# Kernel optimization log

Hardware: AMD Instinct MI355X
Metric: run time of the kernel (lower is better)

Reference implementation:

```python
import jax, jax.numpy as jnp
import numpy as np

N_NODES = 150000
D = 64
N_EDGES = 2000000  # bidirectional: 2 * num_train_edges


def setup_inputs() -> dict:
    key = jax.random.key(0)
    k1, k2, k3, k4, k5 = jax.random.split(key, 5)
    nodes_emb = jax.random.normal(k1, (N_NODES, D), dtype=jnp.float32)
    src = jax.random.randint(k2, (N_EDGES,), 0, N_NODES, dtype=jnp.int64 if jax.config.jax_enable_x64 else jnp.int32).astype(jnp.int32)
    dst = jax.random.randint(k3, (N_EDGES,), 0, N_NODES, dtype=jnp.int32)
    W1 = jax.random.normal(k4, (2 * D, D), dtype=jnp.float32) * (1.0 / np.sqrt(2 * D))
    b1 = jnp.zeros((D,), dtype=jnp.float32)
    W2 = jax.random.normal(k5, (D, 1), dtype=jnp.float32) * (1.0 / np.sqrt(D))
    b2 = jnp.zeros((1,), dtype=jnp.float32)
    return {"nodes_emb": nodes_emb, "src": src, "dst": dst,
            "W1": W1, "b1": b1, "W2": W2, "b2": b2}


def reference(nodes_emb, src, dst, W1, b1, W2, b2):
    # Gather per-edge endpoint embeddings and concat: [E, 2D]
    emb_src = nodes_emb[src]          # [E, D]
    emb_dst = nodes_emb[dst]          # [E, D]
    edge_emb = jnp.concatenate([emb_src, emb_dst], axis=1)  # [E, 2D]
    # 2-layer MLP edge scorer: Linear(2D->D) -> ReLU -> Linear(D->1)
    h = jax.nn.relu(edge_emb @ W1 + b1)  # [E, D]
    edge_logits = h @ W2 + b2            # [E, 1]
    return edge_logits
```

## Files before the change

kernel.cpp:

```cpp
#include <hip/hip_runtime.h>
#include <math.h>

typedef __attribute__((ext_vector_type(8))) short bf16x8;
typedef __attribute__((ext_vector_type(4))) float f32x4;
typedef __attribute__((ext_vector_type(2))) unsigned int u32x2;
typedef __attribute__((ext_vector_type(4))) unsigned int u32x4;
typedef unsigned long long u64;

#define LDSTR 136
#define TPW 8
#define NREP 128
#define NBKT 64

static __device__ __forceinline__ unsigned int pack2bf(float x, float y) {
  unsigned int ux = __builtin_bit_cast(unsigned int, x);
  ux += 0x7fffu + ((ux >> 16) & 1u);
  unsigned int uy = __builtin_bit_cast(unsigned int, y);
  uy += 0x7fffu + ((uy >> 16) & 1u);
  return (ux >> 16) | (uy & 0xffff0000u);
}
static __device__ __forceinline__ unsigned short f2bf_s(float x) {
  unsigned int ux = __builtin_bit_cast(unsigned int, x);
  ux += 0x7fffu + ((ux >> 16) & 1u);
  return (unsigned short)(ux >> 16);
}
static __device__ __forceinline__ bf16x8 make_afrag(float4 lo, float4 hi) {
  u32x4 p;
  p[0] = pack2bf(lo.x, lo.y);
  p[1] = pack2bf(lo.z, lo.w);
  p[2] = pack2bf(hi.x, hi.y);
  p[3] = pack2bf(hi.z, hi.w);
  return __builtin_bit_cast(bf16x8, p);
}

static __device__ __forceinline__ unsigned int q8(float v, float inv) {
  return (unsigned int)((int)rintf(v * inv) + 128);
}

static __device__ __forceinline__ float dot8i(u32x2 P, u32x2 Q, float sp, float sq,
                                              const float* w2v) {
  const float t_ = -128.f * (sp + sq);
  float acc = 0.f;
  #pragma unroll
  for (int k2 = 0; k2 < 2; ++k2) {
    const unsigned int pd = P[k2], qd = Q[k2];
    #pragma unroll
    for (int b = 0; b < 4; ++b) {
      float pf = (float)((pd >> (8 * b)) & 0xffu);
      float qf = (float)((qd >> (8 * b)) & 0xffu);
      float h = __builtin_fmaf(pf, sp, __builtin_fmaf(qf, sq, t_));
      h = fmaxf(h, 0.f);
      acc = __builtin_fmaf(h, w2v[k2 * 4 + b], acc);
    }
  }
  return acc;
}

__global__ __launch_bounds__(256) void node_proj(
    const float* __restrict__ emb,
    const float* __restrict__ W1,
    const float* __restrict__ b1,
    unsigned int* __restrict__ P8,
    unsigned int* __restrict__ Q8,
    float* __restrict__ SP,
    float* __restrict__ SQ,
    int N, int ntiles)
{
  __shared__ unsigned short ls_w1t[64 * LDSTR];
  const int tid  = threadIdx.x;
  const int wave = tid >> 6;
  const int lane = tid & 63;
  const int l15  = lane & 15;
  const int quad = lane >> 4;

  for (int i = tid; i < 64 * 128; i += 256) {
    int k = i >> 6, n = i & 63;
    ls_w1t[n * LDSTR + k] = f2bf_s(W1[i]);
  }
  __syncthreads();

  float b1q[4];
  #pragma unroll
  for (int tn = 0; tn < 4; ++tn) b1q[tn] = b1[tn * 16 + l15];

  bf16x8 bfragP[4][2], bfragQ[4][2];
  #pragma unroll
  for (int tn = 0; tn < 4; ++tn)
    #pragma unroll
    for (int s = 0; s < 2; ++s) {
      bfragP[tn][s] = *(const bf16x8*)&ls_w1t[(tn * 16 + l15) * LDSTR + s * 32 + quad * 8];
      bfragQ[tn][s] = *(const bf16x8*)&ls_w1t[(tn * 16 + l15) * LDSTR + 64 + s * 32 + quad * 8];
    }

  for (int tile = blockIdx.x * 4 + wave; tile < ntiles; tile += gridDim.x * 4) {
    const int base = tile * 16;

    bf16x8 afr0, afr1;
    {
      int node = base + l15;
      node = (node < N) ? node : N - 1;
      const float* rp = emb + (long long)node * 64 + quad * 8;
      afr0 = make_afrag(*(const float4*)(rp),      *(const float4*)(rp + 4));
      afr1 = make_afrag(*(const float4*)(rp + 32), *(const float4*)(rp + 36));
    }

    f32x4 aP[4], aQ[4];
    #pragma unroll
    for (int tn = 0; tn < 4; ++tn) { aP[tn] = (f32x4){0,0,0,0}; aQ[tn] = (f32x4){0,0,0,0}; }
    #pragma unroll
    for (int tn = 0; tn < 4; ++tn) {
      aP[tn] = __builtin_amdgcn_mfma_f32_16x16x32_bf16(afr0, bfragP[tn][0], aP[tn], 0, 0, 0);
      aQ[tn] = __builtin_amdgcn_mfma_f32_16x16x32_bf16(afr0, bfragQ[tn][0], aQ[tn], 0, 0, 0);
      aP[tn] = __builtin_amdgcn_mfma_f32_16x16x32_bf16(afr1, bfragP[tn][1], aP[tn], 0, 0, 0);
      aQ[tn] = __builtin_amdgcn_mfma_f32_16x16x32_bf16(afr1, bfragQ[tn][1], aQ[tn], 0, 0, 0);
    }

    #pragma unroll
    for (int r = 0; r < 4; ++r) {
      const int m = base + quad * 4 + r;
      float vp0 = aP[0][r], vp1 = aP[1][r], vp2 = aP[2][r], vp3 = aP[3][r];
      float vq0 = aQ[0][r] + b1q[0], vq1 = aQ[1][r] + b1q[1];
      float vq2 = aQ[2][r] + b1q[2], vq3 = aQ[3][r] + b1q[3];

      float mp = fmaxf(fmaxf(fabsf(vp0), fabsf(vp1)), fmaxf(fabsf(vp2), fabsf(vp3)));
      float mq = fmaxf(fmaxf(fabsf(vq0), fabsf(vq1)), fmaxf(fabsf(vq2), fabsf(vq3)));
      mp = fmaxf(mp, __shfl_xor(mp, 1)); mq = fmaxf(mq, __shfl_xor(mq, 1));
      mp = fmaxf(mp, __shfl_xor(mp, 2)); mq = fmaxf(mq, __shfl_xor(mq, 2));
      mp = fmaxf(mp, __shfl_xor(mp, 4)); mq = fmaxf(mq, __shfl_xor(mq, 4));
      mp = fmaxf(mp, __shfl_xor(mp, 8)); mq = fmaxf(mq, __shfl_xor(mq, 8));

      const float invP = (mp > 0.f) ? 127.f / mp : 0.f;
      const float invQ = (mq > 0.f) ? 127.f / mq : 0.f;

      if (m < N) {
        unsigned int pw = q8(vp0, invP) | (q8(vp1, invP) << 8) |
                          (q8(vp2, invP) << 16) | (q8(vp3, invP) << 24);
        unsigned int qw = q8(vq0, invQ) | (q8(vq1, invQ) << 8) |
                          (q8(vq2, invQ) << 16) | (q8(vq3, invQ) << 24);
        P8[(long long)m * 16 + l15] = pw;
        Q8[(long long)m * 16 + l15] = qw;
        if (l15 == 0) {
          SP[m] = mp * (1.f / 127.f);
          SQ[m] = mq * (1.f / 127.f);
        }
      }
    }
  }
}

__global__ __launch_bounds__(256) void bucketize(
    const int* __restrict__ src, const int* __restrict__ dst,
    unsigned int* __restrict__ seg, unsigned short* __restrict__ posrec,
    unsigned int* __restrict__ cntT,
    int E, int ndiv, int cap)
{
  __shared__ unsigned int curs[NBKT];
  const int r = blockIdx.x;
  const int per = (E + NREP - 1) / NREP;
  const int lo = r * per;
  const int hi = (lo + per < E) ? lo + per : E;
  for (int i = threadIdx.x; i < NBKT; i += 256) curs[i] = 0;
  __syncthreads();
  for (int e = lo + threadIdx.x; e < hi; e += 256) {
    const int s = src[e], d = dst[e];
    const int bi = s / ndiv, bj = d / ndiv;
    const int bkt = bi * 8 + bj;
    const unsigned int pos = atomicAdd(&curs[bkt], 1u);
    unsigned short pr = 0xFFFFu;
    if (pos < (unsigned)cap) {
      seg[((size_t)(r * NBKT + bkt)) * cap + pos] =
          (unsigned)(s - bi * ndiv) | ((unsigned)(d - bj * ndiv) << 15);
      pr = (unsigned short)(((unsigned)bkt << 9) | pos);
    }
    posrec[e] = pr;
  }
  __syncthreads();
  for (int bkt = threadIdx.x; bkt < NBKT; bkt += 256) {
    unsigned int c = curs[bkt];
    cntT[bkt * NREP + r] = (c < (unsigned)cap) ? c : (unsigned)cap;
  }
}

__global__ __launch_bounds__(256) void edge_score_seg(
    const unsigned int* __restrict__ P8, const unsigned int* __restrict__ Q8,
    const float* __restrict__ SP, const float* __restrict__ SQ,
    const unsigned int* __restrict__ seg, const unsigned int* __restrict__ cntT,
    const float* __restrict__ W2, const float* __restrict__ b2,
    float* __restrict__ tmp, int cap, int ndiv)
{
  const int tid  = threadIdx.x;
  const int lane = tid & 63;
  const int sv   = lane & 7;
  const int g    = lane >> 3;
  const int k    = blockIdx.x & 7;
  const int tblk = blockIdx.x >> 3;
  const int wgid = tblk * 4 + (tid >> 6);
  const int r    = wgid >> 3;
  const int sub  = wgid & 7;

  float w2v[8];
  #pragma unroll
  for (int j = 0; j < 8; ++j) {
    const int pos = sv * 8 + j;
    const int ch  = (pos & 3) * 16 + (pos >> 2);
    w2v[j] = W2[ch];
  }
  const float b2v = b2[0];
  const int sd = sv * 2;
  const int sbase = k * ndiv;

  #pragma unroll 1
  for (int j = 0; j < 8; ++j) {
    const int b = k * 8 + j;
    const int dbase = j * ndiv;
    const int cnt = (int)cntT[b * NREP + r];
    const int chunk = (cnt + 7) >> 3;
    const int lo = sub * chunk;
    const int hi = (cnt < lo + chunk) ? cnt : lo + chunk;
    const unsigned int* sgp = seg + (size_t)(r * NBKT + b) * cap;
    float* tp = tmp + (size_t)(r * NBKT + b) * cap;

    #pragma unroll 2
    for (int m = lo + g; m < hi; m += 8) {
      const unsigned int v = sgp[m];
      const int s_ = sbase + (int)(v & 0x7FFFu);
      const int d_ = dbase + (int)(v >> 15);

      const u32x2 pv = *(const u32x2*)(P8 + s_ * 16 + sd);
      const u32x2 qv = *(const u32x2*)(Q8 + d_ * 16 + sd);
      const float sp = SP[s_], sq = SQ[d_];

      float acc = dot8i(pv, qv, sp, sq, w2v);
      acc += __shfl_xor(acc, 1);
      acc += __shfl_xor(acc, 2);
      acc += __shfl_xor(acc, 4);
      if (sv == 0) tp[m] = acc + b2v;
    }
  }
}

__global__ __launch_bounds__(256) void unscatter(
    const unsigned short* __restrict__ posrec, const float* __restrict__ tmp,
    float* __restrict__ out,
    const int* __restrict__ src, const int* __restrict__ dst,
    const unsigned int* __restrict__ P8, const unsigned int* __restrict__ Q8,
    const float* __restrict__ SP, const float* __restrict__ SQ,
    const float* __restrict__ W2, const float* __restrict__ b2,
    int E, int per, int cap)
{
  const int r   = blockIdx.x >> 3;
  const int sub = blockIdx.x & 7;
  const int lo_r = r * per;
  int lenr = E - lo_r;
  if (lenr <= 0) return;
  if (lenr > per) lenr = per;
  const int chunk = (lenr + 7) >> 3;
  const int lo = lo_r + sub * chunk;
  int hi = lo + chunk;
  const int end_r = lo_r + lenr;
  if (hi > end_r) hi = end_r;
  const float* tb = tmp + (size_t)r * NBKT * cap;

  for (int e = lo + threadIdx.x; e < hi; e += 256) {
    const unsigned int pr = posrec[e];
    if (pr != 0xFFFFu) {
      out[e] = tb[(pr >> 9) * cap + (pr & 511u)];
    } else {
      const int s_ = src[e], d_ = dst[e];
      const float sp = SP[s_], sq = SQ[d_];
      const float t_ = -128.f * (sp + sq);
      float acc = 0.f;
      for (int w = 0; w < 16; ++w) {
        const unsigned int pd = P8[(size_t)s_ * 16 + w];
        const unsigned int qd = Q8[(size_t)d_ * 16 + w];
        for (int bb = 0; bb < 4; ++bb) {
          const int pos = w * 4 + bb;
          const int ch  = (pos & 3) * 16 + (pos >> 2);
          float pf = (float)((pd >> (8 * bb)) & 0xffu);
          float qf = (float)((qd >> (8 * bb)) & 0xffu);
          float h = __builtin_fmaf(pf, sp, __builtin_fmaf(qf, sq, t_));
          h = fmaxf(h, 0.f);
          acc = __builtin_fmaf(h, W2[ch], acc);
        }
      }
      out[e] = acc + b2[0];
    }
  }
}

__global__ __launch_bounds__(256) void edge_score(
    const unsigned int* __restrict__ P8, const unsigned int* __restrict__ Q8,
    const float* __restrict__ SP, const float* __restrict__ SQ,
    const int* __restrict__ src, const int* __restrict__ dst,
    const float* __restrict__ W2, const float* __restrict__ b2,
    float* __restrict__ out, int E)
{
  const int tid  = blockIdx.x * 256 + threadIdx.x;
  const int lane = threadIdx.x & 63;
  const int s    = lane & 7;
  const int g    = lane >> 3;
  const int wid  = tid >> 6;
  const int step = gridDim.x * 4 * 32;

  float w2v[8];
  #pragma unroll
  for (int j = 0; j < 8; ++j) {
    const int pos = s * 8 + j;
    const int ch  = (pos & 3) * 16 + (pos >> 2);
    w2v[j] = W2[ch];
  }
  const float b2v = b2[0];
  const int sd = s * 2;

  int e0 = wid * 32;
  if (e0 >= E) return;

  int iA, iB, iC, iD, jA, jB, jC, jD;
  {
    const int eA = e0 + g,      eAc = (eA < E) ? eA : E - 1;
    const int eB = e0 + 8 + g,  eBc = (eB < E) ? eB : E - 1;
    const int eC = e0 + 16 + g, eCc = (eC < E) ? eC : E - 1;
    const int eD = e0 + 24 + g, eDc = (eD < E) ? eD : E - 1;
    iA = src[eAc]; jA = dst[eAc];
    iB = src[eBc]; jB = dst[eBc];
    iC = src[eCc]; jC = dst[eCc];
    iD = src[eDc]; jD = dst[eDc];
  }
  float spA = SP[iA], sqA = SQ[jA];
  float spB = SP[iB], sqB = SQ[jB];
  float spC = SP[iC], sqC = SQ[jC];
  float spD = SP[iD], sqD = SQ[jD];

  while (true) {
    const u32x2 pA = *(const u32x2*)(P8 + iA * 16 + sd);
    const u32x2 qA = *(const u32x2*)(Q8 + jA * 16 + sd);
    const u32x2 pB = *(const u32x2*)(P8 + iB * 16 + sd);
    const u32x2 qB = *(const u32x2*)(Q8 + jB * 16 + sd);
    const u32x2 pC = *(const u32x2*)(P8 + iC * 16 + sd);
    const u32x2 qC = *(const u32x2*)(Q8 + jC * 16 + sd);
    const u32x2 pD = *(const u32x2*)(P8 + iD * 16 + sd);
    const u32x2 qD = *(const u32x2*)(Q8 + jD * 16 + sd);

    const int en = e0 + step;
    const bool more = (en < E);
    int nA = iA, nB = iB, nC = iC, nD = iD;
    int mA = jA, mB = jB, mC = jC, mD = jD;
    if (more) {
      const int fA = en + g,      fAc = (fA < E) ? fA : E - 1;
      const int fB = en + 8 + g,  fBc = (fB < E) ? fB : E - 1;
      const int fC = en + 16 + g, fCc = (fC < E) ? fC : E - 1;
      const int fD = en + 24 + g, fDc = (fD < E) ? fD : E - 1;
      nA = src[fAc]; mA = dst[fAc];
      nB = src[fBc]; mB = dst[fBc];
      nC = src[fCc]; mC = dst[fCc];
      nD = src[fDc]; mD = dst[fDc];
    }

    float accA = dot8i(pA, qA, spA, sqA, w2v);
    float accB = dot8i(pB, qB, spB, sqB, w2v);
    float accC = dot8i(pC, qC, spC, sqC, w2v);
    float accD = dot8i(pD, qD, spD, sqD, w2v);

    accA += __shfl_xor(accA, 1); accB += __shfl_xor(accB, 1);
    accC += __shfl_xor(accC, 1); accD += __shfl_xor(accD, 1);
    accA += __shfl_xor(accA, 2); accB += __shfl_xor(accB, 2);
    accC += __shfl_xor(accC, 2); accD += __shfl_xor(accD, 2);
    accA += __shfl_xor(accA, 4); accB += __shfl_xor(accB, 4);
    accC += __shfl_xor(accC, 4); accD += __shfl_xor(accD, 4);

    if (s == 0) {
      const int eA = e0 + g;
      const int eB = e0 + 8 + g;
      const int eC = e0 + 16 + g;
      const int eD = e0 + 24 + g;
      if (eA < E) out[eA] = accA + b2v;
      if (eB < E) out[eB] = accB + b2v;
      if (eC < E) out[eC] = accC + b2v;
      if (eD < E) out[eD] = accD + b2v;
    }

    if (!more) break;
    iA = nA; iB = nB; iC = nC; iD = nD;
    jA = mA; jB = mB; jC = mC; jD = mD;
    spA = SP[iA]; sqA = SQ[jA];
    spB = SP[iB]; sqB = SQ[jB];
    spC = SP[iC]; sqC = SQ[jC];
    spD = SP[iD]; sqD = SQ[jD];
    e0 = en;
  }
}

__global__ __launch_bounds__(256) void edge_mlp_f32(
    const float* __restrict__ nodes_emb, const int* __restrict__ src,
    const int* __restrict__ dst, const float* __restrict__ W1,
    const float* __restrict__ b1, const float* __restrict__ W2,
    const float* __restrict__ b2, float* __restrict__ out, int E)
{
  __shared__ unsigned short ls_w1t[64 * LDSTR];
  __shared__ float ls_b1[64];
  __shared__ float ls_w2[64];
  const int tid = threadIdx.x, wave = tid >> 6, lane = tid & 63;
  const int l15 = lane & 15, quad = lane >> 4;
  for (int i = tid; i < 64 * 128; i += 256) {
    int n = i >> 7, k = i & 127;
    ls_w1t[n * LDSTR + k] = f2bf_s(W1[k * 64 + n]);
  }
  if (tid < 64) { ls_b1[tid] = b1[tid]; ls_w2[tid] = W2[tid]; }
  __syncthreads();
  bf16x8 bfrag[4][4];
  #pragma unroll
  for (int tn = 0; tn < 4; ++tn)
    #pragma unroll
    for (int s = 0; s < 4; ++s)
      bfrag[tn][s] = *(const bf16x8*)&ls_w1t[(tn * 16 + l15) * LDSTR + s * 32 + quad * 8];
  float myb1[4], myw2[4];
  #pragma unroll
  for (int tn = 0; tn < 4; ++tn) { myb1[tn] = ls_b1[tn*16+l15]; myw2[tn] = ls_w2[tn*16+l15]; }
  const float b2v = b2[0];
  const int wave_base = blockIdx.x * (TPW * 64) + wave * (TPW * 16);
  #pragma unroll 1
  for (int t = 0; t < TPW; ++t) {
    const int tile_base = wave_base + t * 16;
    if (tile_base >= E) break;
    const int e = tile_base + l15;
    const int si = src[e], di = dst[e];
    const float* srow = nodes_emb + (long long)si * 64 + quad * 8;
    const float* drow = nodes_emb + (long long)di * 64 + quad * 8;
    float4 v0 = *(const float4*)(srow),      v1 = *(const float4*)(srow + 4);
    float4 v2 = *(const float4*)(srow + 32), v3 = *(const float4*)(srow + 36);
    float4 v4 = *(const float4*)(drow),      v5 = *(const float4*)(drow + 4);
    float4 v6 = *(const float4*)(drow + 32), v7 = *(const float4*)(drow + 36);
    bf16x8 afr[4] = {make_afrag(v0,v1), make_afrag(v2,v3), make_afrag(v4,v5), make_afrag(v6,v7)};
    f32x4 acc[4];
    #pragma unroll
    for (int tn = 0; tn < 4; ++tn) acc[tn] = (f32x4){0.f,0.f,0.f,0.f};
    #pragma unroll
    for (int s = 0; s < 4; ++s)
      #pragma unroll
      for (int tn = 0; tn < 4; ++tn)
        acc[tn] = __builtin_amdgcn_mfma_f32_16x16x32_bf16(afr[s], bfrag[tn][s], acc[tn], 0, 0, 0);
    #pragma unroll
    for (int r = 0; r < 4; ++r) {
      float p = 0.f;
      #pragma unroll
      for (int tn = 0; tn < 4; ++tn) {
        float h = fmaxf(acc[tn][r] + myb1[tn], 0.f);
        p = __builtin_fmaf(h, myw2[tn], p);
      }
      p += __shfl_xor(p, 1); p += __shfl_xor(p, 2);
      p += __shfl_xor(p, 4); p += __shfl_xor(p, 8);
      if (l15 == 0) out[tile_base + quad * 4 + r] = p + b2v;
    }
  }
}

extern "C" void kernel_launch(void* const* d_in, const int* in_sizes, int n_in,
                              void* d_out, int out_size, void* d_ws, size_t ws_size,
                              hipStream_t stream) {
  const float* nodes_emb = (const float*)d_in[0];
  const int*   src       = (const int*)d_in[1];
  const int*   dst       = (const int*)d_in[2];
  const float* W1        = (const float*)d_in[3];
  const float* b1        = (const float*)d_in[4];
  const float* W2        = (const float*)d_in[5];
  const float* b2        = (const float*)d_in[6];
  float* out = (float*)d_out;

  const int E = in_sizes[1];
  const int nodes_elems = in_sizes[0];
  const int N = nodes_elems / 64;
  const int ntiles = (N + 15) / 16;
  const int ndiv = (N + 7) / 8;
  const int per  = (E + NREP - 1) / NREP;

  const long long cells = (long long)NBKT * NREP;
  const int perCell = (int)((E + cells - 1) / cells);
  const int sig = (int)ceilf(sqrtf((float)(perCell > 0 ? perCell : 1)));
  const int cap = perCell + 6 * sig + 8;

  const size_t szRow   = (size_t)N * 64;
  const size_t offSP   = szRow * 2;
  const size_t offSQ   = offSP + (size_t)N * 4;
  const size_t offCnt  = offSQ + (size_t)N * 4;
  const size_t offPos  = offCnt + (size_t)NBKT * NREP * 4;
  const size_t offSeg  = (offPos + (size_t)E * 2 + 7) & ~(size_t)7;
  const size_t offTmp  = offSeg + (size_t)NBKT * NREP * (size_t)cap * 4;
  const size_t need_full = offTmp + (size_t)NBKT * NREP * (size_t)cap * 4;
  const size_t need_mid  = offCnt;

  if (ws_size >= need_mid && N > 0) {
    unsigned int* P8 = (unsigned int*)d_ws;
    unsigned int* Q8 = (unsigned int*)((char*)d_ws + szRow);
    float* SP = (float*)((char*)d_ws + offSP);
    float* SQ = (float*)((char*)d_ws + offSQ);
    hipLaunchKernelGGL(node_proj, dim3(512), dim3(256), 0, stream,
                       nodes_emb, W1, b1, P8, Q8, SP, SQ, N, ntiles);
    if (ws_size >= need_full && cap <= 511 && ndiv <= 32767) {
      unsigned int*  cntT   = (unsigned int*)((char*)d_ws + offCnt);
      unsigned short* posrec = (unsigned short*)((char*)d_ws + offPos);
      unsigned int*  seg    = (unsigned int*)((char*)d_ws + offSeg);
      float*         tmp    = (float*)((char*)d_ws + offTmp);
      hipLaunchKernelGGL(bucketize, dim3(NREP), dim3(256), 0, stream,
                         src, dst, seg, posrec, cntT, E, ndiv, cap);
      hipLaunchKernelGGL(edge_score_seg, dim3(2048), dim3(256), 0, stream,
                         P8, Q8, SP, SQ, seg, cntT, W2, b2, tmp, cap, ndiv);
      hipLaunchKernelGGL(unscatter, dim3(NREP * 8), dim3(256), 0, stream,
                         posrec, tmp, out, src, dst, P8, Q8, SP, SQ, W2, b2,
                         E, per, cap);
    } else {
      hipLaunchKernelGGL(edge_score, dim3(4096), dim3(256), 0, stream,
                         P8, Q8, SP, SQ, src, dst, W2, b2, out, E);
    }
  } else {
    const int epb = TPW * 64;
    const int blocks = (E + epb - 1) / epb;
    hipLaunchKernelGGL(edge_mlp_f32, dim3(blocks), dim3(256), 0, stream,
                       nodes_emb, src, dst, W1, b1, W2, b2, out, E);
  }
}
```

Before: 205.8 us.

## Fuse node projection and bucketize into one launch; prefetch next edge in scorer

Merges the independent node_proj and bucketize kernels into a single fused_prep launch, with blocks split by index, so the two phases run concurrently and one launch boundary disappears. The edge scoring loop now software-pipelines its gathers, loading the next edge's P8/Q8/scale values before computing the current one, and it preloads the per-bucket counts into registers. The fused kernel's shared memory footprint is the larger of the two bodies, which may reduce occupancy, and the prefetch raises register pressure.

```diff
diff --git a/kernel.cpp b/kernel.cpp
--- a/kernel.cpp
+++ b/kernel.cpp
@@ -11,6 +11,7 @@
 #define TPW 8
 #define NREP 128
 #define NBKT 64
+#define PROJ_BLOCKS 512
 
 static __device__ __forceinline__ unsigned int pack2bf(float x, float y) {
   unsigned int ux = __builtin_bit_cast(unsigned int, x);
@@ -56,15 +57,12 @@
   return acc;
 }
 
-__global__ __launch_bounds__(256) void node_proj(
-    const float* __restrict__ emb,
-    const float* __restrict__ W1,
+static __device__ void node_proj_body(
+    const float* __restrict__ emb, const float* __restrict__ W1,
     const float* __restrict__ b1,
-    unsigned int* __restrict__ P8,
-    unsigned int* __restrict__ Q8,
-    float* __restrict__ SP,
-    float* __restrict__ SQ,
-    int N, int ntiles)
+    unsigned int* __restrict__ P8, unsigned int* __restrict__ Q8,
+    float* __restrict__ SP, float* __restrict__ SQ,
+    int N, int ntiles, int nblocks, int bid)
 {
   __shared__ unsigned short ls_w1t[64 * LDSTR];
   const int tid  = threadIdx.x;
@@ -92,7 +90,7 @@
       bfragQ[tn][s] = *(const bf16x8*)&ls_w1t[(tn * 16 + l15) * LDSTR + 64 + s * 32 + quad * 8];
     }
 
-  for (int tile = blockIdx.x * 4 + wave; tile < ntiles; tile += gridDim.x * 4) {
+  for (int tile = bid * 4 + wave; tile < ntiles; tile += nblocks * 4) {
     const int base = tile * 16;
 
     bf16x8 afr0, afr1;
@@ -148,14 +146,12 @@
   }
 }
 
-__global__ __launch_bounds__(256) void bucketize(
+static __device__ void bucketize_body(
     const int* __restrict__ src, const int* __restrict__ dst,
     unsigned int* __restrict__ seg, unsigned short* __restrict__ posrec,
-    unsigned int* __restrict__ cntT,
-    int E, int ndiv, int cap)
+    unsigned int* __restrict__ cntT, int E, int ndiv, int cap, int r)
 {
   __shared__ unsigned int curs[NBKT];
-  const int r = blockIdx.x;
   const int per = (E + NREP - 1) / NREP;
   const int lo = r * per;
   const int hi = (lo + per < E) ? lo + per : E;
@@ -181,6 +177,31 @@
   }
 }
 
+__global__ __launch_bounds__(256) void fused_prep(
+    const float* __restrict__ emb, const float* __restrict__ W1,
+    const float* __restrict__ b1,
+    unsigned int* __restrict__ P8, unsigned int* __restrict__ Q8,
+    float* __restrict__ SP, float* __restrict__ SQ,
+    const int* __restrict__ src, const int* __restrict__ dst,
+    unsigned int* __restrict__ seg, unsigned short* __restrict__ posrec,
+    unsigned int* __restrict__ cntT,
+    int N, int ntiles, int E, int ndiv, int cap)
+{
+  if (blockIdx.x < PROJ_BLOCKS)
+    node_proj_body(emb, W1, b1, P8, Q8, SP, SQ, N, ntiles, PROJ_BLOCKS, blockIdx.x);
+  else
+    bucketize_body(src, dst, seg, posrec, cntT, E, ndiv, cap, blockIdx.x - PROJ_BLOCKS);
+}
+
+__global__ __launch_bounds__(256) void node_proj(
+    const float* __restrict__ emb, const float* __restrict__ W1,
+    const float* __restrict__ b1,
+    unsigned int* __restrict__ P8, unsigned int* __restrict__ Q8,
+    float* __restrict__ SP, float* __restrict__ SQ, int N, int ntiles)
+{
+  node_proj_body(emb, W1, b1, P8, Q8, SP, SQ, N, ntiles, gridDim.x, blockIdx.x);
+}
+
 __global__ __launch_bounds__(256) void edge_score_seg(
     const unsigned int* __restrict__ P8, const unsigned int* __restrict__ Q8,
     const float* __restrict__ SP, const float* __restrict__ SQ,
@@ -209,32 +230,52 @@
   const int sd = sv * 2;
   const int sbase = k * ndiv;
 
+  int cnts[8];
+  #pragma unroll
+  for (int j = 0; j < 8; ++j) cnts[j] = (int)cntT[(k * 8 + j) * NREP + r];
+
   #pragma unroll 1
   for (int j = 0; j < 8; ++j) {
     const int b = k * 8 + j;
     const int dbase = j * ndiv;
-    const int cnt = (int)cntT[b * NREP + r];
+    const int cnt = cnts[j];
     const int chunk = (cnt + 7) >> 3;
     const int lo = sub * chunk;
     const int hi = (cnt < lo + chunk) ? cnt : lo + chunk;
     const unsigned int* sgp = seg + (size_t)(r * NBKT + b) * cap;
     float* tp = tmp + (size_t)(r * NBKT + b) * cap;
 
-    #pragma unroll 2
-    for (int m = lo + g; m < hi; m += 8) {
-      const unsigned int v = sgp[m];
-      const int s_ = sbase + (int)(v & 0x7FFFu);
-      const int d_ = dbase + (int)(v >> 15);
-
-      const u32x2 pv = *(const u32x2*)(P8 + s_ * 16 + sd);
-      const u32x2 qv = *(const u32x2*)(Q8 + d_ * 16 + sd);
-      const float sp = SP[s_], sq = SQ[d_];
+    int m = lo + g;
+    if (m >= hi) continue;
+
+    unsigned int v = sgp[m];
+    int s_ = sbase + (int)(v & 0x7FFFu);
+    int d_ = dbase + (int)(v >> 15);
+    u32x2 pv = *(const u32x2*)(P8 + s_ * 16 + sd);
+    u32x2 qv = *(const u32x2*)(Q8 + d_ * 16 + sd);
+    float sp = SP[s_], sq = SQ[d_];
+
+    while (true) {
+      const int m2 = m + 8;
+      const bool more = (m2 < hi);
+      u32x2 pv2, qv2; float sp2 = 0.f, sq2 = 0.f;
+      if (more) {
+        const unsigned int vn = sgp[m2];
+        const int s2 = sbase + (int)(vn & 0x7FFFu);
+        const int d2 = dbase + (int)(vn >> 15);
+        pv2 = *(const u32x2*)(P8 + s2 * 16 + sd);
+        qv2 = *(const u32x2*)(Q8 + d2 * 16 + sd);
+        sp2 = SP[s2]; sq2 = SQ[d2];
+      }
 
       float acc = dot8i(pv, qv, sp, sq, w2v);
       acc += __shfl_xor(acc, 1);
       acc += __shfl_xor(acc, 2);
       acc += __shfl_xor(acc, 4);
       if (sv == 0) tp[m] = acc + b2v;
+
+      if (!more) break;
+      m = m2; pv = pv2; qv = qv2; sp = sp2; sq = sq2;
     }
   }
 }
@@ -493,21 +534,22 @@
     unsigned int* Q8 = (unsigned int*)((char*)d_ws + szRow);
     float* SP = (float*)((char*)d_ws + offSP);
     float* SQ = (float*)((char*)d_ws + offSQ);
-    hipLaunchKernelGGL(node_proj, dim3(512), dim3(256), 0, stream,
-                       nodes_emb, W1, b1, P8, Q8, SP, SQ, N, ntiles);
     if (ws_size >= need_full && cap <= 511 && ndiv <= 32767) {
-      unsigned int*  cntT   = (unsigned int*)((char*)d_ws + offCnt);
+      unsigned int*   cntT   = (unsigned int*)((char*)d_ws + offCnt);
       unsigned short* posrec = (unsigned short*)((char*)d_ws + offPos);
-      unsigned int*  seg    = (unsigned int*)((char*)d_ws + offSeg);
-      float*         tmp    = (float*)((char*)d_ws + offTmp);
-      hipLaunchKernelGGL(bucketize, dim3(NREP), dim3(256), 0, stream,
-                         src, dst, seg, posrec, cntT, E, ndiv, cap);
+      unsigned int*   seg    = (unsigned int*)((char*)d_ws + offSeg);
+      float*          tmp    = (float*)((char*)d_ws + offTmp);
+      hipLaunchKernelGGL(fused_prep, dim3(PROJ_BLOCKS + NREP), dim3(256), 0, stream,
+                         nodes_emb, W1, b1, P8, Q8, SP, SQ,
+                         src, dst, seg, posrec, cntT, N, ntiles, E, ndiv, cap);
       hipLaunchKernelGGL(edge_score_seg, dim3(2048), dim3(256), 0, stream,
                          P8, Q8, SP, SQ, seg, cntT, W2, b2, tmp, cap, ndiv);
       hipLaunchKernelGGL(unscatter, dim3(NREP * 8), dim3(256), 0, stream,
                          posrec, tmp, out, src, dst, P8, Q8, SP, SQ, W2, b2,
                          E, per, cap);
     } else {
+      hipLaunchKernelGGL(node_proj, dim3(512), dim3(256), 0, stream,
+                         nodes_emb, W1, b1, P8, Q8, SP, SQ, N, ntiles);
       hipLaunchKernelGGL(edge_score, dim3(4096), dim3(256), 0, stream,
                          P8, Q8, SP, SQ, src, dst, W2, b2, out, E);
     }
```

Result: no change. 206.6 us (+0.4%).

## Pack per-node scales into bucket records and unroll bucketize edge loop

Applied to the files above, without the earlier changes.

Bucketize now gathers the SP/SQ scales for each edge and stores them as bf16 next to the packed index pair, in an 8-byte record. This moves the scattered scale loads out of edge_score_seg and into the sequential bucketing pass. The bucketize loop is unrolled four ways so several src/dst loads and scale gathers are in flight at once. edge_score_seg also preloads its bucket counts and skips empty ranges, and the overflow capacity margin is reduced. In exchange, the segment buffer doubles in size, the scales lose precision by rounding to bf16, and the tighter capacity raises the chance of overflow into the fallback path.

```diff
diff --git a/kernel.cpp b/kernel.cpp
--- a/kernel.cpp
+++ b/kernel.cpp
@@ -57,14 +57,10 @@
 }
 
 __global__ __launch_bounds__(256) void node_proj(
-    const float* __restrict__ emb,
-    const float* __restrict__ W1,
+    const float* __restrict__ emb, const float* __restrict__ W1,
     const float* __restrict__ b1,
-    unsigned int* __restrict__ P8,
-    unsigned int* __restrict__ Q8,
-    float* __restrict__ SP,
-    float* __restrict__ SQ,
-    int N, int ntiles)
+    unsigned int* __restrict__ P8, unsigned int* __restrict__ Q8,
+    float* __restrict__ SP, float* __restrict__ SQ, int N, int ntiles)
 {
   __shared__ unsigned short ls_w1t[64 * LDSTR];
   const int tid  = threadIdx.x;
@@ -150,9 +146,9 @@
 
 __global__ __launch_bounds__(256) void bucketize(
     const int* __restrict__ src, const int* __restrict__ dst,
-    unsigned int* __restrict__ seg, unsigned short* __restrict__ posrec,
-    unsigned int* __restrict__ cntT,
-    int E, int ndiv, int cap)
+    const float* __restrict__ SP, const float* __restrict__ SQ,
+    u32x2* __restrict__ seg, unsigned short* __restrict__ posrec,
+    unsigned int* __restrict__ cntT, int E, int ndiv, int cap)
 {
   __shared__ unsigned int curs[NBKT];
   const int r = blockIdx.x;
@@ -161,18 +157,43 @@
   const int hi = (lo + per < E) ? lo + per : E;
   for (int i = threadIdx.x; i < NBKT; i += 256) curs[i] = 0;
   __syncthreads();
-  for (int e = lo + threadIdx.x; e < hi; e += 256) {
-    const int s = src[e], d = dst[e];
-    const int bi = s / ndiv, bj = d / ndiv;
-    const int bkt = bi * 8 + bj;
-    const unsigned int pos = atomicAdd(&curs[bkt], 1u);
-    unsigned short pr = 0xFFFFu;
-    if (pos < (unsigned)cap) {
-      seg[((size_t)(r * NBKT + bkt)) * cap + pos] =
-          (unsigned)(s - bi * ndiv) | ((unsigned)(d - bj * ndiv) << 15);
-      pr = (unsigned short)(((unsigned)bkt << 9) | pos);
-    }
-    posrec[e] = pr;
+
+  for (int e0 = lo + threadIdx.x; e0 < hi; e0 += 1024) {
+    const int e1 = e0 + 256, e2 = e0 + 512, e3 = e0 + 768;
+    const int e1c = (e1 < hi) ? e1 : hi - 1;
+    const int e2c = (e2 < hi) ? e2 : hi - 1;
+    const int e3c = (e3 < hi) ? e3 : hi - 1;
+    const int s0 = src[e0],  d0 = dst[e0];
+    const int s1 = src[e1c], d1 = dst[e1c];
+    const int s2 = src[e2c], d2 = dst[e2c];
+    const int s3 = src[e3c], d3 = dst[e3c];
+    const float sp0 = SP[s0], sq0 = SQ[d0];
+    const float sp1 = SP[s1], sq1 = SQ[d1];
+    const float sp2 = SP[s2], sq2 = SQ[d2];
+    const float sp3 = SP[s3], sq3 = SQ[d3];
+
+#define BK_PROC(EE, SS, DD, SPV, SQV)                                         \
+    {                                                                         \
+      const int bi = (SS) / ndiv, bj = (DD) / ndiv;                           \
+      const int bkt = bi * 8 + bj;                                            \
+      const unsigned int pos = atomicAdd(&curs[bkt], 1u);                     \
+      unsigned short pr = 0xFFFFu;                                            \
+      if (pos < (unsigned)cap) {                                              \
+        u32x2 ev;                                                             \
+        ev[0] = (unsigned)((SS) - bi * ndiv) |                                \
+                ((unsigned)((DD) - bj * ndiv) << 15);                         \
+        ev[1] = ((unsigned)f2bf_s(SPV) << 16) | (unsigned)f2bf_s(SQV);        \
+        seg[((size_t)(r * NBKT + bkt)) * cap + pos] = ev;                     \
+        pr = (unsigned short)(((unsigned)bkt << 9) | pos);                    \
+      }                                                                       \
+      posrec[EE] = pr;                                                        \
+    }
+
+    BK_PROC(e0, s0, d0, sp0, sq0);
+    if (e1 < hi) BK_PROC(e1, s1, d1, sp1, sq1);
+    if (e2 < hi) BK_PROC(e2, s2, d2, sp2, sq2);
+    if (e3 < hi) BK_PROC(e3, s3, d3, sp3, sq3);
+#undef BK_PROC
   }
   __syncthreads();
   for (int bkt = threadIdx.x; bkt < NBKT; bkt += 256) {
@@ -183,8 +204,7 @@
 
 __global__ __launch_bounds__(256) void edge_score_seg(
     const unsigned int* __restrict__ P8, const unsigned int* __restrict__ Q8,
-    const float* __restrict__ SP, const float* __restrict__ SQ,
-    const unsigned int* __restrict__ seg, const unsigned int* __restrict__ cntT,
+    const u32x2* __restrict__ seg, const unsigned int* __restrict__ cntT,
     const float* __restrict__ W2, const float* __restrict__ b2,
     float* __restrict__ tmp, int cap, int ndiv)
 {
@@ -209,26 +229,32 @@
   const int sd = sv * 2;
   const int sbase = k * ndiv;
 
+  int cnts[8];
+  #pragma unroll
+  for (int j = 0; j < 8; ++j) cnts[j] = (int)cntT[(k * 8 + j) * NREP + r];
+
   #pragma unroll 1
   for (int j = 0; j < 8; ++j) {
     const int b = k * 8 + j;
     const int dbase = j * ndiv;
-    const int cnt = (int)cntT[b * NREP + r];
+    const int cnt = cnts[j];
     const int chunk = (cnt + 7) >> 3;
     const int lo = sub * chunk;
     const int hi = (cnt < lo + chunk) ? cnt : lo + chunk;
-    const unsigned int* sgp = seg + (size_t)(r * NBKT + b) * cap;
+    if (lo >= hi) continue;
+    const u32x2* sgp = seg + (size_t)(r * NBKT + b) * cap;
     float* tp = tmp + (size_t)(r * NBKT + b) * cap;
 
     #pragma unroll 2
     for (int m = lo + g; m < hi; m += 8) {
-      const unsigned int v = sgp[m];
-      const int s_ = sbase + (int)(v & 0x7FFFu);
-      const int d_ = dbase + (int)(v >> 15);
+      const u32x2 v = sgp[m];
+      const int s_ = sbase + (int)(v[0] & 0x7FFFu);
+      const int d_ = dbase + (int)(v[0] >> 15);
+      const float sp = __builtin_bit_cast(float, v[1] & 0xffff0000u);
+      const float sq = __builtin_bit_cast(float, v[1] << 16);
 
       const u32x2 pv = *(const u32x2*)(P8 + s_ * 16 + sd);
       const u32x2 qv = *(const u32x2*)(Q8 + d_ * 16 + sd);
-      const float sp = SP[s_], sq = SQ[d_];
 
       float acc = dot8i(pv, qv, sp, sq, w2v);
       acc += __shfl_xor(acc, 1);
@@ -476,7 +502,7 @@
   const long long cells = (long long)NBKT * NREP;
   const int perCell = (int)((E + cells - 1) / cells);
   const int sig = (int)ceilf(sqrtf((float)(perCell > 0 ? perCell : 1)));
-  const int cap = perCell + 6 * sig + 8;
+  const int cap = perCell + 5 * sig + 8;
 
   const size_t szRow   = (size_t)N * 64;
   const size_t offSP   = szRow * 2;
@@ -484,7 +510,7 @@
   const size_t offCnt  = offSQ + (size_t)N * 4;
   const size_t offPos  = offCnt + (size_t)NBKT * NREP * 4;
   const size_t offSeg  = (offPos + (size_t)E * 2 + 7) & ~(size_t)7;
-  const size_t offTmp  = offSeg + (size_t)NBKT * NREP * (size_t)cap * 4;
+  const size_t offTmp  = offSeg + (size_t)NBKT * NREP * (size_t)cap * 8;
   const size_t need_full = offTmp + (size_t)NBKT * NREP * (size_t)cap * 4;
   const size_t need_mid  = offCnt;
 
@@ -496,14 +522,14 @@
     hipLaunchKernelGGL(node_proj, dim3(512), dim3(256), 0, stream,
                        nodes_emb, W1, b1, P8, Q8, SP, SQ, N, ntiles);
     if (ws_size >= need_full && cap <= 511 && ndiv <= 32767) {
-      unsigned int*  cntT   = (unsigned int*)((char*)d_ws + offCnt);
+      unsigned int*   cntT   = (unsigned int*)((char*)d_ws + offCnt);
       unsigned short* posrec = (unsigned short*)((char*)d_ws + offPos);
-      unsigned int*  seg    = (unsigned int*)((char*)d_ws + offSeg);
-      float*         tmp    = (float*)((char*)d_ws + offTmp);
+      u32x2*          seg    = (u32x2*)((char*)d_ws + offSeg);
+      float*          tmp    = (float*)((char*)d_ws + offTmp);
       hipLaunchKernelGGL(bucketize, dim3(NREP), dim3(256), 0, stream,
-                         src, dst, seg, posrec, cntT, E, ndiv, cap);
+                         src, dst, SP, SQ, seg, posrec, cntT, E, ndiv, cap);
       hipLaunchKernelGGL(edge_score_seg, dim3(2048), dim3(256), 0, stream,
-                         P8, Q8, SP, SQ, seg, cntT, W2, b2, tmp, cap, ndiv);
+                         P8, Q8, seg, cntT, W2, b2, tmp, cap, ndiv);
       hipLaunchKernelGGL(unscatter, dim3(NREP * 8), dim3(256), 0, stream,
                          posrec, tmp, out, src, dst, P8, Q8, SP, SQ, W2, b2,
                          E, per, cap);
```

New measurement: 206.9 us. No clear change (+0.5%).
